# Optimization experiments

Measured on AMD Instinct MI355X. Metric: run time of the kernel, lower is better.

Reference implementation:

```python
import jax, jax.numpy as jnp
import numpy as np

B, C, L, H, W = 4, 96, 32, 56, 56
KD = 16
NUM_SCALES = 2  # 1 + ceil(log2(L / KD)) for L=32, KD=16


def setup_inputs() -> dict:
    key = jax.random.key(0)
    ks = jax.random.split(key, 5)
    x = jax.random.normal(ks[0], (B, C, L, H, W), jnp.float32)
    width_conv = jax.random.normal(ks[1], (C, W), jnp.float32)
    height_conv = jax.random.normal(ks[2], (C, H), jnp.float32)
    kernel0 = jax.random.normal(ks[3], (1, C, KD), jnp.float32)
    kernel1 = jax.random.normal(ks[4], (1, C, KD), jnp.float32)
    # decay init: rand*(decay_max-decay_min)+decay_min == 2.0 exactly (min==max==2)
    decay = jnp.full((1, C, 1), 2.0, jnp.float32)
    return dict(x=x, width_conv=width_conv, height_conv=height_conv,
                kernel0=kernel0, kernel1=kernel1, decay=decay)


def _interp_linear(k, scale):
    """F.interpolate(k, scale_factor=scale, mode='linear', align_corners=False)."""
    if scale == 1:
        return k
    Lk = k.shape[-1]
    out_len = Lk * scale
    src = jnp.maximum((jnp.arange(out_len, dtype=jnp.float32) + 0.5) / scale - 0.5, 0.0)
    lo = jnp.floor(src).astype(jnp.int32)
    frac = src - lo.astype(jnp.float32)
    hi = jnp.minimum(lo + 1, Lk - 1)
    return k[..., lo] * (1.0 - frac) + k[..., hi] * frac


def _fftconv(x, kf, axis, n, out_len):
    # causal FFT conv with zero-padding to n=2*dim, truncated back to out_len
    xf = jnp.fft.rfft(x, n=n, axis=axis)
    y = jnp.fft.irfft(xf * kf, n=n, axis=axis)
    return jax.lax.slice_in_dim(y, 0, out_len, axis=axis)


def _length_kernel(kernel0, kernel1, decay):
    parts = []
    for i, kern in enumerate((kernel0, kernel1)):
        ki = _interp_linear(kern, 2 ** i) * decay ** (NUM_SCALES - i - 1)
        parts.append(ki)
    k = jnp.concatenate(parts, axis=-1)[0, :, :L]            # (C, L)
    norm = jax.lax.stop_gradient(jnp.linalg.norm(k, axis=-1, keepdims=True))
    return k / norm


def reference(x, width_conv, height_conv, kernel0, kernel1, decay):
    # x: (B, C, L, H, W). The torch rearranges are pure layout moves; the math is
    # a per-channel 1D FFT conv along W, then H, then L.
    kf_w = jnp.fft.rfft(width_conv, n=2 * W)                 # (C, W+1)
    x = _fftconv(x, kf_w[None, :, None, None, :], axis=4, n=2 * W, out_len=W)
    kf_h = jnp.fft.rfft(height_conv, n=2 * H)                # (C, H+1)
    x = _fftconv(x, kf_h[None, :, None, :, None], axis=3, n=2 * H, out_len=H)
    k = _length_kernel(kernel0, kernel1, decay)              # (C, L)
    kf_l = jnp.fft.rfft(k, n=2 * L)                          # (C, L+1)
    x = _fftconv(x, kf_l[None, :, :, None, None], axis=2, n=2 * L, out_len=L)
    return x
```

## Files before the change

kernel.cpp:

```cpp
#include <hip/hip_runtime.h>

#define BB 4
#define CC 96
#define LL 32
#define HH 56
#define WW 56
#define HW (HH * WW)
#define KD 16

__global__ __launch_bounds__(256) void conv_wh(const float* __restrict__ x,
                                               const float* __restrict__ wconv,
                                               const float* __restrict__ hconv,
                                               float* __restrict__ out) {
    __shared__ float sl[4][HH][WW + 1];
    __shared__ float wk[WW];
    __shared__ float hk[HH];

    const int tid  = threadIdx.x;
    const int wv   = tid >> 6;
    const int lane = tid & 63;
    const int slice0 = blockIdx.x * 4;
    const int c      = (slice0 / LL) % CC;

    if (tid < WW)                      wk[tid]      = wconv[c * WW + tid];
    else if (tid >= 64 && tid < 64+HH) hk[tid - 64] = hconv[c * HH + (tid - 64)];

    const size_t base = (size_t)(slice0 + wv) * HW;
    #pragma unroll
    for (int i = 0; i < HW / 64; ++i) {
        int m = i * 64 + lane;
        sl[wv][m / WW][m % WW] = x[base + m];
    }
    __syncthreads();

    float xr[HH], acc[HH];

    if (lane < HH) {
        #pragma unroll
        for (int j = 0; j < WW; ++j) xr[j] = sl[wv][lane][j];
        #pragma unroll
        for (int j = 0; j < WW; ++j) acc[j] = 0.f;
        #pragma unroll
        for (int d = 0; d < WW; ++d) {
            const float kd = wk[d];
            #pragma unroll
            for (int w = d; w < WW; ++w)
                acc[w] = fmaf(kd, xr[w - d], acc[w]);
        }
        #pragma unroll
        for (int j = 0; j < WW; ++j) sl[wv][lane][j] = acc[j];
    }
    __syncthreads();

    if (lane < WW) {
        #pragma unroll
        for (int h = 0; h < HH; ++h) xr[h] = sl[wv][h][lane];
        #pragma unroll
        for (int h = 0; h < HH; ++h) acc[h] = 0.f;
        #pragma unroll
        for (int d = 0; d < HH; ++d) {
            const float kd = hk[d];
            #pragma unroll
            for (int h = d; h < HH; ++h)
                acc[h] = fmaf(kd, xr[h - d], acc[h]);
        }
        #pragma unroll
        for (int h = 0; h < HH; ++h)
            out[base + (size_t)h * WW + lane] = acc[h];
    }
}

__global__ __launch_bounds__(256) void conv_l(float* __restrict__ y,
                                              const float* __restrict__ k0,
                                              const float* __restrict__ k1,
                                              const float* __restrict__ decay) {
    __shared__ float kl[LL];
    __shared__ float s_norm;

    const int tid = threadIdx.x;
    const int bc  = blockIdx.y;
    const int c   = bc % CC;

    if (tid < LL) {
        float v;
        const float dec = decay[c];
        if (tid < KD) {
            v = k0[c * KD + tid] * dec;
        } else {
            const int   i    = tid - KD;
            const float src  = fmaxf((i + 0.5f) * 0.5f - 0.5f, 0.f);
            const int   lo   = (int)floorf(src);
            const float frac = src - (float)lo;
            const int   hi   = min(lo + 1, KD - 1);
            v = k1[c * KD + lo] * (1.f - frac) + k1[c * KD + hi] * frac;
        }
        kl[tid] = v;
    }
    __syncthreads();
    if (tid == 0) {
        float s = 0.f;
        for (int i = 0; i < LL; ++i) s += kl[i] * kl[i];
        s_norm = sqrtf(s);
    }
    __syncthreads();

    const float inv = 1.0f / s_norm;
    float kr[LL];
    #pragma unroll
    for (int i = 0; i < LL; ++i) kr[i] = kl[i] * inv;

    const int pos = blockIdx.x * 256 + tid;
    if (pos >= HW) return;

    float* col = y + (size_t)bc * LL * HW + pos;
    float xin[LL];
    #pragma unroll
    for (int l = 0; l < LL; ++l) xin[l] = col[(size_t)l * HW];

    #pragma unroll
    for (int l = LL - 1; l >= 0; --l) {
        float t = 0.f;
        #pragma unroll
        for (int j = 0; j <= l; ++j)
            t = fmaf(kr[l - j], xin[j], t);
        xin[l] = t;
    }
    #pragma unroll
    for (int l = 0; l < LL; ++l) col[(size_t)l * HW] = xin[l];
}

extern "C" void kernel_launch(void* const* d_in, const int* in_sizes, int n_in,
                              void* d_out, int out_size, void* d_ws, size_t ws_size,
                              hipStream_t stream) {
    const float* x     = (const float*)d_in[0];
    const float* wconv = (const float*)d_in[1];
    const float* hconv = (const float*)d_in[2];
    const float* k0    = (const float*)d_in[3];
    const float* k1    = (const float*)d_in[4];
    const float* dec   = (const float*)d_in[5];
    float*       out   = (float*)d_out;

    conv_wh<<<dim3(BB * CC * LL / 4), 256, 0, stream>>>(x, wconv, hconv, out);
    conv_l<<<dim3((HW + 255) / 256, BB * CC), 256, 0, stream>>>(out, k0, k1, dec);
}
```

Measured before the change: 337.5 us.

## Tile W/H causal convolutions into 14-wide chunks to cut register pressure

```diff
diff --git a/kernel.cpp b/kernel.cpp
--- a/kernel.cpp
+++ b/kernel.cpp
@@ -7,23 +7,21 @@
 #define WW 56
 #define HW (HH * WW)
 #define KD 16
+#define CH 14
 
-__global__ __launch_bounds__(256) void conv_wh(const float* __restrict__ x,
-                                               const float* __restrict__ wconv,
-                                               const float* __restrict__ hconv,
-                                               float* __restrict__ out) {
+__global__ __launch_bounds__(256, 3) void conv_wh(const float* __restrict__ x,
+                                                  const float* __restrict__ wconv,
+                                                  const float* __restrict__ hconv,
+                                                  float* __restrict__ out) {
     __shared__ float sl[4][HH][WW + 1];
-    __shared__ float wk[WW];
-    __shared__ float hk[HH];
 
     const int tid  = threadIdx.x;
     const int wv   = tid >> 6;
     const int lane = tid & 63;
     const int slice0 = blockIdx.x * 4;
     const int c      = (slice0 / LL) % CC;
-
-    if (tid < WW)                      wk[tid]      = wconv[c * WW + tid];
-    else if (tid >= 64 && tid < 64+HH) hk[tid - 64] = hconv[c * HH + (tid - 64)];
+    const float* __restrict__ kw = wconv + c * WW;
+    const float* __restrict__ kh = hconv + c * HH;
 
     const size_t base = (size_t)(slice0 + wv) * HW;
     #pragma unroll
@@ -33,47 +31,98 @@
     }
     __syncthreads();
 
-    float xr[HH], acc[HH];
-
     if (lane < HH) {
+        float* row = &sl[wv][lane][0];
         #pragma unroll
-        for (int j = 0; j < WW; ++j) xr[j] = sl[wv][lane][j];
-        #pragma unroll
-        for (int j = 0; j < WW; ++j) acc[j] = 0.f;
-        #pragma unroll
-        for (int d = 0; d < WW; ++d) {
-            const float kd = wk[d];
+        for (int t = 3; t >= 0; --t) {
+            const int w0 = t * CH;
+            float acc[CH];
             #pragma unroll
-            for (int w = d; w < WW; ++w)
-                acc[w] = fmaf(kd, xr[w - d], acc[w]);
+            for (int i = 0; i < CH; ++i) acc[i] = 0.f;
+            #pragma unroll
+            for (int u = 0; u < t; ++u) {
+                const int u0 = u * CH;
+                float xch[CH];
+                #pragma unroll
+                for (int j = 0; j < CH; ++j) xch[j] = row[u0 + j];
+                #pragma unroll
+                for (int dd = 0; dd < 2 * CH - 1; ++dd) {
+                    const float kd = kw[w0 - u0 - (CH - 1) + dd];
+                    const int delta = dd - (CH - 1);
+                    #pragma unroll
+                    for (int j = 0; j < CH; ++j) {
+                        const int i = j + delta;
+                        if (i >= 0 && i < CH)
+                            acc[i] = fmaf(kd, xch[j], acc[i]);
+                    }
+                }
+            }
+            {
+                float xch[CH];
+                #pragma unroll
+                for (int j = 0; j < CH; ++j) xch[j] = row[w0 + j];
+                #pragma unroll
+                for (int dd = 0; dd < CH; ++dd) {
+                    const float kd = kw[dd];
+                    #pragma unroll
+                    for (int j = 0; j < CH - dd; ++j)
+                        acc[j + dd] = fmaf(kd, xch[j], acc[j + dd]);
+                }
+            }
+            #pragma unroll
+            for (int i = 0; i < CH; ++i) row[w0 + i] = acc[i];
         }
-        #pragma unroll
-        for (int j = 0; j < WW; ++j) sl[wv][lane][j] = acc[j];
     }
     __syncthreads();
 
     if (lane < WW) {
         #pragma unroll
-        for (int h = 0; h < HH; ++h) xr[h] = sl[wv][h][lane];
-        #pragma unroll
-        for (int h = 0; h < HH; ++h) acc[h] = 0.f;
-        #pragma unroll
-        for (int d = 0; d < HH; ++d) {
-            const float kd = hk[d];
+        for (int t = 3; t >= 0; --t) {
+            const int h0 = t * CH;
+            float acc[CH];
             #pragma unroll
-            for (int h = d; h < HH; ++h)
-                acc[h] = fmaf(kd, xr[h - d], acc[h]);
+            for (int i = 0; i < CH; ++i) acc[i] = 0.f;
+            #pragma unroll
+            for (int u = 0; u < t; ++u) {
+                const int u0 = u * CH;
+                float xch[CH];
+                #pragma unroll
+                for (int j = 0; j < CH; ++j) xch[j] = sl[wv][u0 + j][lane];
+                #pragma unroll
+                for (int dd = 0; dd < 2 * CH - 1; ++dd) {
+                    const float kd = kh[h0 - u0 - (CH - 1) + dd];
+                    const int delta = dd - (CH - 1);
+                    #pragma unroll
+                    for (int j = 0; j < CH; ++j) {
+                        const int i = j + delta;
+                        if (i >= 0 && i < CH)
+                            acc[i] = fmaf(kd, xch[j], acc[i]);
+                    }
+                }
+            }
+            {
+                float xch[CH];
+                #pragma unroll
+                for (int j = 0; j < CH; ++j) xch[j] = sl[wv][h0 + j][lane];
+                #pragma unroll
+                for (int dd = 0; dd < CH; ++dd) {
+                    const float kd = kh[dd];
+                    #pragma unroll
+                    for (int j = 0; j < CH - dd; ++j)
+                        acc[j + dd] = fmaf(kd, xch[j], acc[j + dd]);
+                }
+            }
+            #pragma unroll
+            for (int i = 0; i < CH; ++i)
+                out[base + (size_t)(h0 + i) * WW + lane] = acc[i];
         }
-        #pragma unroll
-        for (int h = 0; h < HH; ++h)
-            out[base + (size_t)h * WW + lane] = acc[h];
     }
 }
 
-__global__ __launch_bounds__(256) void conv_l(float* __restrict__ y,
-                                              const float* __restrict__ k0,
-                                              const float* __restrict__ k1,
-                                              const float* __restrict__ decay) {
+__global__ __launch_bounds__(256, 2) void conv_l(float* __restrict__ y,
+                                                 const float* __restrict__ k0,
+                                                 const float* __restrict__ k1,
+                                                 const float* __restrict__ decay) {
     __shared__ float kl[LL];
     __shared__ float s_norm;
 
```

Result: no change. 342.2 us (+1.4%).
